# Kernel tuning notes

Hardware: AMD Instinct MI355X
Metric: run time of the kernel (lower is better)

Reference implementation:

```python
import jax, jax.numpy as jnp
import numpy as np

B, S, D = 4, 2048, 1024
H, DH = 16, 64

def setup_inputs() -> dict:
    key = jax.random.key(0)
    kx, kq, kk, kv, ko = jax.random.split(key, 5)
    scale = 1.0 / np.sqrt(D)
    return {
        "x": jax.random.normal(kx, (B, S, D), dtype=jnp.float32),
        "Wq": jax.random.normal(kq, (D, H * DH), dtype=jnp.float32) * scale,
        "Wk": jax.random.normal(kk, (D, H * DH), dtype=jnp.float32) * scale,
        "Wv": jax.random.normal(kv, (D, H * DH), dtype=jnp.float32) * scale,
        "Wo": jax.random.normal(ko, (H * DH, D), dtype=jnp.float32) * scale,
    }

def reference(x, Wq, Wk, Wv, Wo):
    b, s, _ = x.shape
    # projections -> [b, h, s, dh]
    q = (x @ Wq).reshape(b, s, H, DH).transpose(0, 2, 1, 3)
    k = (x @ Wk).reshape(b, s, H, DH).transpose(0, 2, 1, 3)
    v = (x @ Wv).reshape(b, s, H, DH).transpose(0, 2, 1, 3)
    logits = jnp.einsum("bhqd,bhkd->bhqk", q, k) / jnp.sqrt(jnp.float32(DH))
    # mask = triu(ones, diagonal=1): True above diagonal -> masked
    mask = jnp.triu(jnp.ones((s, s), dtype=bool), k=1)
    logits = jnp.where(mask, -jnp.inf, logits)
    probs = jax.nn.softmax(logits, axis=-1)
    attn = jnp.einsum("bhqk,bhkd->bhqd", probs, v)
    attn = attn.transpose(0, 2, 1, 3).reshape(b, s, H * DH)
    return attn @ Wo
```

## Files before the change

### kernel.cpp

```cpp
#include <hip/hip_runtime.h>
#include <stdint.h>

#define NB 4
#define NS 2048
#define ND 1024
#define NH 16
#define NDH 64

typedef __attribute__((ext_vector_type(8))) short bf16x8;
typedef __attribute__((ext_vector_type(4))) float f32x4;
typedef __attribute__((ext_vector_type(2))) unsigned int u32x2;

#define MFMA16(a, b, c) __builtin_amdgcn_mfma_f32_16x16x32_bf16((a), (b), (c), 0, 0, 0)

__device__ __forceinline__ uint16_t f2bf(float f) {
  uint32_t u = __builtin_bit_cast(uint32_t, f);
  return (uint16_t)((u + 0x7FFFu + ((u >> 16) & 1u)) >> 16);
}

__device__ __forceinline__ uint32_t pk2(float lo, float hi) {
  return (__builtin_bit_cast(uint32_t, hi) & 0xFFFF0000u) |
         (__builtin_bit_cast(uint32_t, lo) >> 16);
}

__device__ __forceinline__ void gload_lds16(const void* g, void* l) {
  __builtin_amdgcn_global_load_lds(
      (const __attribute__((address_space(1))) uint32_t*)(uintptr_t)g,
      (__attribute__((address_space(3))) uint32_t*)(uintptr_t)l, 16, 0, 0);
}

__global__ __launch_bounds__(256) void prep_kernel(const float* __restrict__ x,
                                                   const float* __restrict__ Wq,
                                                   const float* __restrict__ Wk,
                                                   const float* __restrict__ Wv,
                                                   const float* __restrict__ Wo,
                                                   uint16_t* __restrict__ xb,
                                                   uint16_t* __restrict__ Wt3,
                                                   uint16_t* __restrict__ Wot) {
  const int bid = blockIdx.x;
  if (bid < 4096) {
    __shared__ uint16_t tile[32][33];
    const int which = bid >> 10;
    const int tl = bid & 1023;
    const int bx = (tl & 31) * 32;
    const int by = (tl >> 5) * 32;
    const int tx = threadIdx.x & 31;
    const int ty = threadIdx.x >> 5;
    const float* W = (which == 0) ? Wq : (which == 1) ? Wk : (which == 2) ? Wv : Wo;
    uint16_t* Wt = (which < 3) ? (Wt3 + (size_t)which * (1u << 20)) : Wot;
#pragma unroll
    for (int j = 0; j < 4; j++)
      tile[ty + j * 8][tx] = f2bf(W[(size_t)(by + ty + j * 8) * 1024 + bx + tx]);
    __syncthreads();
#pragma unroll
    for (int j = 0; j < 4; j++)
      Wt[(size_t)(bx + ty + j * 8) * 1024 + by + tx] = tile[tx][ty + j * 8];
  } else {
    const int i = (bid - 4096) * 256 + threadIdx.x;
    const float4 f = *(const float4*)(x + (size_t)i * 4);
    union { uint16_t u[4]; uint64_t q; } o;
    o.u[0] = f2bf(f.x); o.u[1] = f2bf(f.y); o.u[2] = f2bf(f.z); o.u[3] = f2bf(f.w);
    *(uint64_t*)(xb + (size_t)i * 4) = o.q;
  }
}

template <int MODE, int NBX>
__global__ __launch_bounds__(256) void gemm_bt(const uint16_t* __restrict__ A,
                                               const uint16_t* __restrict__ Bt,
                                               uint16_t* __restrict__ O0,
                                               uint16_t* __restrict__ O1,
                                               uint16_t* __restrict__ O2,
                                               float* __restrict__ OF) {
  __shared__ uint16_t lds[2][2][128 * 64];
  const int tid = threadIdx.x;
  const int lane = tid & 63;
  const int wave = tid >> 6;
  const int wr = wave >> 1, wc = wave & 1;
  const int l15 = lane & 15, lg = lane >> 4;

  const int nwg = NBX * 64;
  const int wg = ((int)blockIdx.x & 7) * (nwg >> 3) + ((int)blockIdx.x >> 3);
  const int st = wg >> 5, in32 = wg & 31;
  const int sy = in32 >> 2, sx = in32 & 3;
  const int stx = st % (NBX / 4), sty = st / (NBX / 4);
  const int row0 = (sty * 8 + sy) * 128;
  const int col0 = (stx * 4 + sx) * 128;

  f32x4 acc[4][4];
#pragma unroll
  for (int i = 0; i < 4; i++)
#pragma unroll
    for (int j = 0; j < 4; j++) acc[i][j] = f32x4{0.f, 0.f, 0.f, 0.f};

  const char* Ag = (const char*)A + (size_t)row0 * 2048;
  const char* Bg = (const char*)Bt + (size_t)col0 * 2048;

  const int srr = tid >> 3;
  const int csrc = ((tid & 7) - srr) & 7;

#define STAGE_TILE(buf, t)                                                          \
  {                                                                                 \
    char* la = (char*)&lds[buf][0][0] + wave * 1024;                                \
    char* lb = (char*)&lds[buf][1][0] + wave * 1024;                                \
    _Pragma("unroll") for (int j = 0; j < 4; ++j) {                                 \
      const size_t off = (size_t)(j * 32 + srr) * 2048 + (size_t)(t) * 128 + csrc * 16; \
      gload_lds16(Ag + off, la + j * 4096);                                         \
      gload_lds16(Bg + off, lb + j * 4096);                                         \
    }                                                                               \
  }

  STAGE_TILE(0, 0);
  __syncthreads();

  int cur = 0;
  for (int t = 0; t < 16; ++t) {
    if (t < 15) STAGE_TILE(cur ^ 1, t + 1);
    const char* cA = (const char*)&lds[cur][0][0];
    const char* cB = (const char*)&lds[cur][1][0];
    bf16x8 af[4][2], bfr[4][2];
#pragma unroll
    for (int mi = 0; mi < 4; mi++) {
      const int row = wr * 64 + mi * 16 + l15;
#pragma unroll
      for (int ks = 0; ks < 2; ks++) {
        const int ch = (ks * 4 + lg + (l15 & 7)) & 7;
        af[mi][ks] = *(const bf16x8*)(cA + row * 128 + ch * 16);
      }
    }
#pragma unroll
    for (int ni = 0; ni < 4; ni++) {
      const int row = wc * 64 + ni * 16 + l15;
#pragma unroll
      for (int ks = 0; ks < 2; ks++) {
        const int ch = (ks * 4 + lg + (l15 & 7)) & 7;
        bfr[ni][ks] = *(const bf16x8*)(cB + row * 128 + ch * 16);
      }
    }
#pragma unroll
    for (int ks = 0; ks < 2; ks++)
#pragma unroll
      for (int mi = 0; mi < 4; mi++)
#pragma unroll
        for (int ni = 0; ni < 4; ni++)
          acc[mi][ni] = MFMA16(af[mi][ks], bfr[ni][ks], acc[mi][ni]);
    __syncthreads();
    cur ^= 1;
  }

#pragma unroll
  for (int mi = 0; mi < 4; mi++) {
#pragma unroll
    for (int ni = 0; ni < 4; ni++) {
      const int c = col0 + wc * 64 + ni * 16 + l15;
      const int rbase = row0 + wr * 64 + mi * 16 + lg * 4;
#pragma unroll
      for (int i = 0; i < 4; i++) {
        const int r = rbase + i;
        const float v = acc[mi][ni][i];
        if (MODE == 0) {
          const int which = c >> 10, cc = c & 1023;
          const int h = cc >> 6, dh = cc & 63;
          const int b = r >> 11, s = r & 2047;
          const size_t hb = (size_t)(b * NH + h);
          if (which == 0)
            O0[(hb * NS + s) * 64 + dh] = f2bf(v * 0.18033688011112042f);
          else if (which == 1)
            O1[(hb * NS + s) * 64 + dh] = f2bf(v);
          else
            O2[(((hb * 32 + (s >> 6)) * 64 + dh) * 64) + (s & 63)] = f2bf(v);
        } else {
          OF[(size_t)r * 1024 + c] = v;
        }
      }
    }
  }
#undef STAGE_TILE
}

__device__ __forceinline__ void stage_kv(const char* __restrict__ Kg,
                                         const char* __restrict__ Vg,
                                         char* kl, char* vl, int lane) {
#pragma unroll
  for (int j = 0; j < 8; ++j) {
    const int y = j * 1024 + lane * 16;
    const int r = y >> 7;
    const int zs = (r << 7) | ((((y >> 4) - r) & 7) << 4);
    gload_lds16(Kg + zs, kl + j * 1024);
    gload_lds16(Vg + zs, vl + j * 1024);
  }
}

__device__ __forceinline__ void attn_unit(const uint16_t* __restrict__ Qh,
                                          const char* __restrict__ Kg,
                                          const char* __restrict__ Vg,
                                          uint16_t* __restrict__ Aout,
                                          int b, int h, int gp, int l15, int lg, int lane,
                                          char* kl, char* vl,
                                          uint16_t (*pX)[64][16]) {
  const int qbA = gp * 32;
  const int qbB = qbA + 16;
  const int tmax = gp >> 1;
  const int nfdA = (2 * gp) & 3;
  const int nfdB = nfdA + 1;

  stage_kv(Kg, Vg, kl, vl, lane);

  const bf16x8 qfA0 = *(const bf16x8*)&Qh[(size_t)(qbA + l15) * 64 + lg * 8];
  const bf16x8 qfA1 = *(const bf16x8*)&Qh[(size_t)(qbA + l15) * 64 + 32 + lg * 8];
  const bf16x8 qfB0 = *(const bf16x8*)&Qh[(size_t)(qbB + l15) * 64 + lg * 8];
  const bf16x8 qfB1 = *(const bf16x8*)&Qh[(size_t)(qbB + l15) * 64 + 32 + lg * 8];

  const short one_bf = (short)0x3F80;
  const bf16x8 ones = {one_bf, one_bf, one_bf, one_bf, one_bf, one_bf, one_bf, one_bf};

  const int rsw = l15 & 7;

  const int wcol = ((lg + (l15 >> 2)) & 3) * 4;
  const int rr = l15 >> 2, cc0 = l15 & 3;
  const int rot = (2 * lg) & 3;
  const uint32_t pb = (uint32_t)(uintptr_t)&pX[0][0][0];
  const uint32_t addr0 = pb + (uint32_t)(lg * 256 + rr * 32 + (((cc0 + rot) & 3) * 8));
  const uint32_t addr1 = pb + (uint32_t)(lg * 256 + 128 + rr * 32 + (((cc0 + rot + 1) & 3) * 8));

  f32x4 oA[4], oB[4];
  f32x4 rsA = f32x4{0.f, 0.f, 0.f, 0.f};
  f32x4 rsB = f32x4{0.f, 0.f, 0.f, 0.f};
#pragma unroll
  for (int i = 0; i < 4; i++) {
    oA[i] = f32x4{0.f, 0.f, 0.f, 0.f};
    oB[i] = f32x4{0.f, 0.f, 0.f, 0.f};
  }

  for (int t = 0; t <= tmax; ++t) {
    asm volatile("s_waitcnt vmcnt(0)" ::: "memory");
    bf16x8 kf[4][2], vf[4][2];
#pragma unroll
    for (int nf = 0; nf < 4; ++nf)
#pragma unroll
      for (int kk = 0; kk < 2; ++kk) {
        const int off = (nf * 16 + l15) * 128 + (((kk * 4 + lg) + rsw) & 7) * 16;
        kf[nf][kk] = *(const bf16x8*)(kl + off);
        vf[nf][kk] = *(const bf16x8*)(vl + off);
      }
    asm volatile("s_waitcnt lgkmcnt(0)" ::: "memory");
    if (t < tmax) stage_kv(Kg + (size_t)(t + 1) * 8192, Vg + (size_t)(t + 1) * 8192, kl, vl, lane);

    const int nfmA = (t == tmax) ? nfdA : 3;
    const int nfmB = (t == tmax) ? nfdB : 3;
#pragma unroll
    for (int nf = 0; nf < 4; ++nf) {
      if (nf <= nfmB) {
        f32x4 a = f32x4{0.f, 0.f, 0.f, 0.f};
        a = MFMA16(qfB0, kf[nf][0], a);
        a = MFMA16(qfB1, kf[nf][1], a);
        if (t == tmax && nf == nfdB) {
#pragma unroll
          for (int i = 0; i < 4; i++)
            if (l15 > lg * 4 + i) a[i] = -1e30f;
        }
        {
          const float e0 = exp2f(a[0]), e1 = exp2f(a[1]);
          const float e2 = exp2f(a[2]), e3 = exp2f(a[3]);
          *(uint64_t*)&pX[1][nf * 16 + l15][wcol] =
              ((uint64_t)pk2(e2, e3) << 32) | pk2(e0, e1);
        }
        if (nf <= nfmA) {
          f32x4 c = f32x4{0.f, 0.f, 0.f, 0.f};
          c = MFMA16(qfA0, kf[nf][0], c);
          c = MFMA16(qfA1, kf[nf][1], c);
          if (t == tmax && nf == nfdA) {
#pragma unroll
            for (int i = 0; i < 4; i++)
              if (l15 > lg * 4 + i) c[i] = -1e30f;
          }
          const float e0 = exp2f(c[0]), e1 = exp2f(c[1]);
          const float e2 = exp2f(c[2]), e3 = exp2f(c[3]);
          *(uint64_t*)&pX[0][nf * 16 + l15][wcol] =
              ((uint64_t)pk2(e2, e3) << 32) | pk2(e0, e1);
        } else {
          *(uint64_t*)&pX[0][nf * 16 + l15][wcol] = 0ull;
        }
      } else {
        *(uint64_t*)&pX[0][nf * 16 + l15][wcol] = 0ull;
        *(uint64_t*)&pX[1][nf * 16 + l15][wcol] = 0ull;
      }
    }
    u32x2 a0, a1, a2, a3, b0, b1, b2, b3;
    asm volatile(
        "ds_read_b64_tr_b16 %0, %8\n\t"
        "ds_read_b64_tr_b16 %1, %9\n\t"
        "ds_read_b64_tr_b16 %2, %8 offset:1024\n\t"
        "ds_read_b64_tr_b16 %3, %9 offset:1024\n\t"
        "ds_read_b64_tr_b16 %4, %8 offset:2048\n\t"
        "ds_read_b64_tr_b16 %5, %9 offset:2048\n\t"
        "ds_read_b64_tr_b16 %6, %8 offset:3072\n\t"
        "ds_read_b64_tr_b16 %7, %9 offset:3072\n\t"
        "s_waitcnt lgkmcnt(0)"
        : "=&v"(a0), "=&v"(a1), "=&v"(a2), "=&v"(a3),
          "=&v"(b0), "=&v"(b1), "=&v"(b2), "=&v"(b3)
        : "v"(addr0), "v"(addr1)
        : "memory");
    union { u32x2 u2[2]; bf16x8 v8; } uA0, uA1, uB0, uB1;
    uA0.u2[0] = a0; uA0.u2[1] = a1;
    uA1.u2[0] = a2; uA1.u2[1] = a3;
    uB0.u2[0] = b0; uB0.u2[1] = b1;
    uB1.u2[0] = b2; uB1.u2[1] = b3;
    const bf16x8 paA0 = uA0.v8, paA1 = uA1.v8;
    const bf16x8 paB0 = uB0.v8, paB1 = uB1.v8;
    __builtin_amdgcn_s_setprio(1);
    rsA = MFMA16(paA0, ones, rsA);
    rsA = MFMA16(paA1, ones, rsA);
    rsB = MFMA16(paB0, ones, rsB);
    rsB = MFMA16(paB1, ones, rsB);
#pragma unroll
    for (int df = 0; df < 4; ++df) {
      oA[df] = MFMA16(paA0, vf[df][0], oA[df]);
      oA[df] = MFMA16(paA1, vf[df][1], oA[df]);
      oB[df] = MFMA16(paB0, vf[df][0], oB[df]);
      oB[df] = MFMA16(paB1, vf[df][1], oB[df]);
    }
    __builtin_amdgcn_s_setprio(0);
  }

#pragma unroll
  for (int df = 0; df < 4; ++df) {
#pragma unroll
    for (int i = 0; i < 4; i++) {
      const int qA = qbA + lg * 4 + i;
      const int qB = qbB + lg * 4 + i;
      Aout[((size_t)(b * NS + qA)) * 1024 + h * 64 + df * 16 + l15] = f2bf(oA[df][i] / rsA[i]);
      Aout[((size_t)(b * NS + qB)) * 1024 + h * 64 + df * 16 + l15] = f2bf(oB[df][i] / rsB[i]);
    }
  }
}

__global__ __launch_bounds__(256) void attn_fwd(const uint16_t* __restrict__ Q,
                                                const uint16_t* __restrict__ K,
                                                const uint16_t* __restrict__ Vt,
                                                uint16_t* __restrict__ Aout) {
  const int bid = blockIdx.x;
  const int xcd = bid & 7;
  const int sp = (bid >> 3) & 3;
  const int gblk = bid >> 5;

  const int w = threadIdx.x >> 6;
  const int lane = threadIdx.x & 63;
  const int l15 = lane & 15, lg = lane >> 4;
  const int g = gblk * 4 + w;

  __shared__ __align__(16) uint16_t plds[4][2][64][16];
  __shared__ __align__(16) char kstage[4][8192];
  __shared__ __align__(16) char vstage[4][8192];

  for (int seg = 0; seg < 2; ++seg) {
    const int slot = sp * 2 + seg;
    const int bh = (slot << 3) | xcd;
    const int gp = seg ? (63 - g) : g;
    const uint16_t* Qh = Q + (size_t)bh * (NS * 64);
    const char* Kg = (const char*)(K + (size_t)bh * (NS * 64));
    const char* Vg = (const char*)(Vt + (size_t)bh * (32 * 64 * 64));
    attn_unit(Qh, Kg, Vg, Aout, bh >> 4, bh & 15, gp, l15, lg, lane,
              kstage[w], vstage[w], plds[w]);
  }
}

extern "C" void kernel_launch(void* const* d_in, const int* in_sizes, int n_in,
                              void* d_out, int out_size, void* d_ws, size_t ws_size,
                              hipStream_t stream) {
  const float* x = (const float*)d_in[0];
  const float* Wq = (const float*)d_in[1];
  const float* Wk = (const float*)d_in[2];
  const float* Wv = (const float*)d_in[3];
  const float* Wo = (const float*)d_in[4];
  float* out = (float*)d_out;

  char* ws = (char*)d_ws;
  uint16_t* xb = (uint16_t*)(ws);
  uint16_t* Wt3 = (uint16_t*)(ws + (16u << 20));
  uint16_t* Wot = (uint16_t*)(ws + (22u << 20));
  uint16_t* Qb = (uint16_t*)(ws + (24u << 20));
  uint16_t* Kb = (uint16_t*)(ws + (40u << 20));
  uint16_t* Vt = (uint16_t*)(ws + (56u << 20));
  uint16_t* attn = xb;

  prep_kernel<<<12288, 256, 0, stream>>>(x, Wq, Wk, Wv, Wo, xb, Wt3, Wot);

  gemm_bt<0, 24><<<1536, 256, 0, stream>>>(xb, Wt3, Qb, Kb, Vt, nullptr);
  attn_fwd<<<512, 256, 0, stream>>>(Qb, Kb, Vt, attn);
  gemm_bt<1, 8><<<512, 256, 0, stream>>>(attn, Wot, nullptr, nullptr, nullptr, out);
}
```

Measured before the change: 182.9 us.

## Enlarge GEMM tiles to 256x256 with 512 threads and triple-buffered LDS pipeline

Both projection GEMMs now use 256x256 output tiles computed by 8 waves, each wave owning a 128x64 sub-tile. The K step drops to 32 and staging moves to a three-buffer ring, synchronised by explicit vmcnt waits and barriers so two tiles are in flight. The goal is higher arithmetic intensity and better hiding of global-to-LDS latency. In exchange, grids shrink to 384 and 128 blocks, which may underfill the GPU, and LDS and register use per block grow.

```diff
diff --git a/kernel.cpp b/kernel.cpp
--- a/kernel.cpp
+++ b/kernel.cpp
@@ -65,94 +65,93 @@
 }
 
 template <int MODE, int NBX>
-__global__ __launch_bounds__(256) void gemm_bt(const uint16_t* __restrict__ A,
+__global__ __launch_bounds__(512) void gemm_bt(const uint16_t* __restrict__ A,
                                                const uint16_t* __restrict__ Bt,
                                                uint16_t* __restrict__ O0,
                                                uint16_t* __restrict__ O1,
                                                uint16_t* __restrict__ O2,
                                                float* __restrict__ OF) {
-  __shared__ uint16_t lds[2][2][128 * 64];
+  __shared__ uint16_t lds[3][2][256 * 32];
   const int tid = threadIdx.x;
   const int lane = tid & 63;
   const int wave = tid >> 6;
-  const int wr = wave >> 1, wc = wave & 1;
+  const int wr = wave >> 2;
+  const int wn = wave & 3;
   const int l15 = lane & 15, lg = lane >> 4;
 
-  const int nwg = NBX * 64;
+  const int nwg = 32 * NBX;
   const int wg = ((int)blockIdx.x & 7) * (nwg >> 3) + ((int)blockIdx.x >> 3);
   const int st = wg >> 5, in32 = wg & 31;
   const int sy = in32 >> 2, sx = in32 & 3;
   const int stx = st % (NBX / 4), sty = st / (NBX / 4);
-  const int row0 = (sty * 8 + sy) * 128;
-  const int col0 = (stx * 4 + sx) * 128;
-
-  f32x4 acc[4][4];
-#pragma unroll
-  for (int i = 0; i < 4; i++)
+  const int row0 = (sty * 8 + sy) * 256;
+  const int col0 = (stx * 4 + sx) * 256;
+
+  f32x4 acc[8][4];
+#pragma unroll
+  for (int i = 0; i < 8; i++)
 #pragma unroll
     for (int j = 0; j < 4; j++) acc[i][j] = f32x4{0.f, 0.f, 0.f, 0.f};
 
   const char* Ag = (const char*)A + (size_t)row0 * 2048;
   const char* Bg = (const char*)Bt + (size_t)col0 * 2048;
-
-  const int srr = tid >> 3;
-  const int csrc = ((tid & 7) - srr) & 7;
-
-#define STAGE_TILE(buf, t)                                                          \
-  {                                                                                 \
-    char* la = (char*)&lds[buf][0][0] + wave * 1024;                                \
-    char* lb = (char*)&lds[buf][1][0] + wave * 1024;                                \
-    _Pragma("unroll") for (int j = 0; j < 4; ++j) {                                 \
-      const size_t off = (size_t)(j * 32 + srr) * 2048 + (size_t)(t) * 128 + csrc * 16; \
-      gload_lds16(Ag + off, la + j * 4096);                                         \
-      gload_lds16(Bg + off, lb + j * 4096);                                         \
-    }                                                                               \
+  char* ldsbase = (char*)&lds[0][0][0];
+
+  const int srr = tid >> 2;
+  const int csrc = ((tid & 3) - (srr & 3)) & 3;
+
+#define STAGE_TILE(bs, t)                                                              \
+  {                                                                                    \
+    char* la = ldsbase + (bs) * 32768 + wave * 1024;                                   \
+    char* lb = la + 16384;                                                             \
+    _Pragma("unroll") for (int j = 0; j < 2; ++j) {                                    \
+      const size_t off = (size_t)(j * 128 + srr) * 2048 + (size_t)(t) * 64 + csrc * 16;\
+      gload_lds16(Ag + off, la + j * 8192);                                            \
+      gload_lds16(Bg + off, lb + j * 8192);                                            \
+    }                                                                                  \
+  }
+
+#define COMPUTE_TILE(bc)                                                               \
+  {                                                                                    \
+    const char* cA = ldsbase + (bc) * 32768;                                           \
+    const char* cB = cA + 16384;                                                       \
+    bf16x8 af[8], bfr[4];                                                              \
+    _Pragma("unroll") for (int ni = 0; ni < 4; ni++) {                                 \
+      const int row = wn * 64 + ni * 16 + l15;                                         \
+      bfr[ni] = *(const bf16x8*)(cB + row * 64 + ((lg + row) & 3) * 16);               \
+    }                                                                                  \
+    _Pragma("unroll") for (int mi = 0; mi < 8; mi++) {                                 \
+      const int row = wr * 128 + mi * 16 + l15;                                        \
+      af[mi] = *(const bf16x8*)(cA + row * 64 + ((lg + row) & 3) * 16);                \
+    }                                                                                  \
+    _Pragma("unroll") for (int mi = 0; mi < 8; mi++)                                   \
+      _Pragma("unroll") for (int ni = 0; ni < 4; ni++)                                 \
+        acc[mi][ni] = MFMA16(af[mi], bfr[ni], acc[mi][ni]);                            \
   }
 
   STAGE_TILE(0, 0);
-  __syncthreads();
-
-  int cur = 0;
-  for (int t = 0; t < 16; ++t) {
-    if (t < 15) STAGE_TILE(cur ^ 1, t + 1);
-    const char* cA = (const char*)&lds[cur][0][0];
-    const char* cB = (const char*)&lds[cur][1][0];
-    bf16x8 af[4][2], bfr[4][2];
-#pragma unroll
-    for (int mi = 0; mi < 4; mi++) {
-      const int row = wr * 64 + mi * 16 + l15;
-#pragma unroll
-      for (int ks = 0; ks < 2; ks++) {
-        const int ch = (ks * 4 + lg + (l15 & 7)) & 7;
-        af[mi][ks] = *(const bf16x8*)(cA + row * 128 + ch * 16);
-      }
-    }
+  STAGE_TILE(1, 1);
+
+  int bc = 0;
+#pragma unroll 1
+  for (int t = 0; t < 31; ++t) {
+    asm volatile("s_waitcnt vmcnt(4)\n\ts_barrier" ::: "memory");
+    if (t < 30) {
+      int bs = bc + 2; if (bs >= 3) bs -= 3;
+      STAGE_TILE(bs, t + 2);
+    }
+    COMPUTE_TILE(bc);
+    if (++bc == 3) bc = 0;
+  }
+  asm volatile("s_waitcnt vmcnt(0)\n\ts_barrier" ::: "memory");
+  COMPUTE_TILE(bc);
+
+#pragma unroll
+  for (int mi = 0; mi < 8; mi++) {
 #pragma unroll
     for (int ni = 0; ni < 4; ni++) {
-      const int row = wc * 64 + ni * 16 + l15;
-#pragma unroll
-      for (int ks = 0; ks < 2; ks++) {
-        const int ch = (ks * 4 + lg + (l15 & 7)) & 7;
-        bfr[ni][ks] = *(const bf16x8*)(cB + row * 128 + ch * 16);
-      }
-    }
-#pragma unroll
-    for (int ks = 0; ks < 2; ks++)
-#pragma unroll
-      for (int mi = 0; mi < 4; mi++)
-#pragma unroll
-        for (int ni = 0; ni < 4; ni++)
-          acc[mi][ni] = MFMA16(af[mi][ks], bfr[ni][ks], acc[mi][ni]);
-    __syncthreads();
-    cur ^= 1;
-  }
-
-#pragma unroll
-  for (int mi = 0; mi < 4; mi++) {
-#pragma unroll
-    for (int ni = 0; ni < 4; ni++) {
-      const int c = col0 + wc * 64 + ni * 16 + l15;
-      const int rbase = row0 + wr * 64 + mi * 16 + lg * 4;
+      const int c = col0 + wn * 64 + ni * 16 + l15;
+      const int rbase = row0 + wr * 128 + mi * 16 + lg * 4;
 #pragma unroll
       for (int i = 0; i < 4; i++) {
         const int r = rbase + i;
@@ -175,6 +174,7 @@
     }
   }
 #undef STAGE_TILE
+#undef COMPUTE_TILE
 }
 
 __device__ __forceinline__ void stage_kv(const char* __restrict__ Kg,
@@ -385,7 +385,7 @@
 
   prep_kernel<<<12288, 256, 0, stream>>>(x, Wq, Wk, Wv, Wo, xb, Wt3, Wot);
 
-  gemm_bt<0, 24><<<1536, 256, 0, stream>>>(xb, Wt3, Qb, Kb, Vt, nullptr);
+  gemm_bt<0, 12><<<384, 512, 0, stream>>>(xb, Wt3, Qb, Kb, Vt, nullptr);
   attn_fwd<<<512, 256, 0, stream>>>(Qb, Kb, Vt, attn);
-  gemm_bt<1, 8><<<512, 256, 0, stream>>>(attn, Wot, nullptr, nullptr, nullptr, out);
-}
+  gemm_bt<1, 4><<<128, 512, 0, stream>>>(attn, Wot, nullptr, nullptr, nullptr, out);
+}
```

Result: slower. 212.1 us (+16.0%).
